# Optimization experiments

Hardware: AMD Instinct MI355X
Metric: run time of the kernel (lower is better)

## Reference

```python
import jax, jax.numpy as jnp
import numpy as np

T = 4096  # input sequence length; H = T - 16 after convs+pool


def setup_inputs() -> dict:
    key = jax.random.key(0)
    ks = jax.random.split(key, 20)
    def rn(k, shape, scale=0.05):
        return jax.random.normal(k, shape, dtype=jnp.float32) * scale
    return dict(
        evaluation=rn(ks[0], (T, 128), 1.0),
        template=rn(ks[1], (T, 128), 1.0),
        conv1_w=rn(ks[2], (16, 1, 5, 5)),  conv1_b=rn(ks[3], (16,)),
        conv2_w=rn(ks[4], (32, 16, 5, 5)), conv2_b=rn(ks[5], (32,)),
        conv3_w=rn(ks[6], (64, 32, 5, 5)), conv3_b=rn(ks[7], (64,)),
        lin1_w=rn(ks[8], (64, 3712)),      lin1_b=rn(ks[9], (64,)),
        gru_wih=rn(ks[10], (192, 64)),     gru_whh=rn(ks[11], (192, 64)),
        gru_bih=rn(ks[12], (192,)),        gru_bhh=rn(ks[13], (192,)),
        attn_w=rn(ks[14], (1, 64)),        attn_b=rn(ks[15], (1,)),
        lin3_w=rn(ks[16], (128, 64)),      lin3_b=rn(ks[17], (128,)),
        cls_w=rn(ks[18], (2, 128)),        cls_b=rn(ks[19], (2,)),
    )


def _conv(x, w, b):
    y = jax.lax.conv_general_dilated(x, w, (1, 1), 'VALID',
                                     dimension_numbers=('NCHW', 'OIHW', 'NCHW'))
    return y + b[None, :, None, None]


def _encode(x, c1w, c1b, c2w, c2b, c3w, c3b, l1w, l1b, wih, whh, bih, bhh):
    # x: (T, 128) -> (1, 1, T, 128); no activations between convs (as in source)
    x = x.reshape(1, 1, T, 128)
    x = _conv(x, c1w, c1b)   # (1,16,T-4,124)
    x = _conv(x, c2w, c2b)   # (1,32,T-8,120)
    x = _conv(x, c3w, c3b)   # (1,64,T-12,116)
    x = jax.lax.reduce_window(x, -jnp.inf, jax.lax.max,
                              (1, 1, 5, 2), (1, 1, 1, 2), 'VALID')  # (1,64,H,58)
    H = x.shape[2]
    # faithful raw reshape (channel-major flatten), same as torch.reshape
    x = x.reshape(H, 3712)
    x = x @ l1w.T + l1b      # (H, 64)
    # GRU (torch gate order r,z,n), h0 = 0; input gates precomputed
    gi = x @ wih.T + bih     # (H, 192)
    def step(h, gi_t):
        gh = whh @ h + bhh
        ir, iz, inn = jnp.split(gi_t, 3)
        hr, hz, hn = jnp.split(gh, 3)
        r = jax.nn.sigmoid(ir + hr)
        z = jax.nn.sigmoid(iz + hz)
        n = jnp.tanh(inn + r * hn)
        h_new = (1.0 - z) * n + z * h
        return h_new, h_new
    _, out = jax.lax.scan(step, jnp.zeros((64,), dtype=x.dtype), gi)
    return out               # (H, 64)


def reference(evaluation, template, conv1_w, conv1_b, conv2_w, conv2_b,
              conv3_w, conv3_b, lin1_w, lin1_b, gru_wih, gru_whh, gru_bih,
              gru_bhh, attn_w, attn_b, lin3_w, lin3_b, cls_w, cls_b):
    enc = lambda x: _encode(x, conv1_w, conv1_b, conv2_w, conv2_b, conv3_w,
                            conv3_b, lin1_w, lin1_b, gru_wih, gru_whh,
                            gru_bih, gru_bhh)
    e = enc(evaluation)      # (H, 64)
    t = enc(template)        # (H, 64)
    # alignment: aw[m,n] = <e_m, t_n>, softmax over dim 0 (m)
    aw = jax.nn.softmax(e @ t.T, axis=0)      # (H, H)
    t_prim = aw @ t                            # (H, 64)
    distance = jnp.abs(t_prim - e)             # (H, 64)
    attn = jax.nn.softmax((e @ attn_w.T + attn_b).ravel(), axis=0)  # (H,)
    # NOTE: source loops n over distance.size(dim=1)==64, i.e. only the first
    # 64 rows of distance / first 64 attention weights are used (replicated).
    D = distance.shape[1]
    representation = distance[:D].T @ attn[:D]  # (64,)
    out = jax.nn.relu(representation)
    out = jax.nn.relu(out @ lin3_w.T + lin3_b)
    return out @ cls_w.T + cls_b               # (2,)
```

## Files before the change

### kernel.cpp

```cpp
#include <hip/hip_runtime.h>
#include <hip/hip_fp16.h>

constexpr int T_IN = 4096, W_IN = 128;
constexpr int H1 = 4092, W1 = 124, C1 = 16;
constexpr int H2 = 4088, W2 = 120, C2 = 32;
constexpr int H3 = 4084, W3 = 116, C3 = 64;
constexpr int HP = 4080, WPW = 58;
constexpr int KF = 3712;

typedef float f32x16 __attribute__((ext_vector_type(16)));
typedef _Float16 f16x16 __attribute__((ext_vector_type(16)));
typedef _Float16 half2_t __attribute__((ext_vector_type(2)));

#define LOAD25(SRC, W) \
    float p00=(SRC)[0],        p01=(SRC)[1],        p02=(SRC)[2],        p03=(SRC)[3],        p04=(SRC)[4]; \
    float p10=(SRC)[(W)],      p11=(SRC)[(W)+1],    p12=(SRC)[(W)+2],    p13=(SRC)[(W)+3],    p14=(SRC)[(W)+4]; \
    float p20=(SRC)[2*(W)],    p21=(SRC)[2*(W)+1],  p22=(SRC)[2*(W)+2],  p23=(SRC)[2*(W)+3],  p24=(SRC)[2*(W)+4]; \
    float p30=(SRC)[3*(W)],    p31=(SRC)[3*(W)+1],  p32=(SRC)[3*(W)+2],  p33=(SRC)[3*(W)+3],  p34=(SRC)[3*(W)+4]; \
    float p40=(SRC)[4*(W)],    p41=(SRC)[4*(W)+1],  p42=(SRC)[4*(W)+2],  p43=(SRC)[4*(W)+3],  p44=(SRC)[4*(W)+4];

#define TAPS25(T) \
    T(p00, 0)  T(p01, 1)  T(p02, 2)  T(p03, 3)  T(p04, 4) \
    T(p10, 5)  T(p11, 6)  T(p12, 7)  T(p13, 8)  T(p14, 9) \
    T(p20,10)  T(p21,11)  T(p22,12)  T(p23,13)  T(p24,14) \
    T(p30,15)  T(p31,16)  T(p32,17)  T(p33,18)  T(p34,19) \
    T(p40,20)  T(p41,21)  T(p42,22)  T(p43,23)  T(p44,24)

#define KSTEP16(PK, WPTR) do { \
    const float4* w4_ = (const float4*)(WPTR); \
    float4 wA_ = w4_[0], wB_ = w4_[1], wC_ = w4_[2], wD_ = w4_[3]; \
    a0.x = fmaf((PK), wA_.x, a0.x); a0.y = fmaf((PK), wA_.y, a0.y); \
    a0.z = fmaf((PK), wA_.z, a0.z); a0.w = fmaf((PK), wA_.w, a0.w); \
    a1.x = fmaf((PK), wB_.x, a1.x); a1.y = fmaf((PK), wB_.y, a1.y); \
    a1.z = fmaf((PK), wB_.z, a1.z); a1.w = fmaf((PK), wB_.w, a1.w); \
    a2.x = fmaf((PK), wC_.x, a2.x); a2.y = fmaf((PK), wC_.y, a2.y); \
    a2.z = fmaf((PK), wC_.z, a2.z); a2.w = fmaf((PK), wC_.w, a2.w); \
    a3.x = fmaf((PK), wD_.x, a3.x); a3.y = fmaf((PK), wD_.y, a3.y); \
    a3.z = fmaf((PK), wD_.z, a3.z); a3.w = fmaf((PK), wD_.w, a3.w); \
} while (0)

__global__ __launch_bounds__(256, 2) void conv1_k(const float* __restrict__ x,
        const float* __restrict__ wp, const float* __restrict__ b,
        float* __restrict__ out) {
    int pos = blockIdx.x * 256 + threadIdx.x;
    if (pos >= H1 * W1) return;
    int h = pos / W1, wi = pos - h * W1;
    const float* src = x + h * W_IN + wi;
    const float4* b4 = (const float4*)b;
    float4 a0 = b4[0], a1 = b4[1], a2 = b4[2], a3 = b4[3];
    LOAD25(src, W_IN);
#define T1(P, K) KSTEP16(P, wp + (K) * 16);
    TAPS25(T1)
#undef T1
#pragma unroll
    for (int i = 0; i < 4; i++) {
        float4 v = (i == 0) ? a0 : (i == 1) ? a1 : (i == 2) ? a2 : a3;
        out[(size_t)(i * 4 + 0) * (H1 * W1) + pos] = v.x;
        out[(size_t)(i * 4 + 1) * (H1 * W1) + pos] = v.y;
        out[(size_t)(i * 4 + 2) * (H1 * W1) + pos] = v.z;
        out[(size_t)(i * 4 + 3) * (H1 * W1) + pos] = v.w;
    }
}

__global__ __launch_bounds__(256, 2) void conv2_k(const float* __restrict__ in,
        const float* __restrict__ wp, const float* __restrict__ b,
        float* __restrict__ out) {
    int pos = blockIdx.x * 256 + threadIdx.x;
    if (pos >= H2 * W2) return;
    int co0 = blockIdx.y * 16;
    int h = pos / W2, wi = pos - h * W2;
    const float4* b4 = (const float4*)(b + co0);
    float4 a0 = b4[0], a1 = b4[1], a2 = b4[2], a3 = b4[3];
#pragma unroll 1
    for (int ci = 0; ci < C1; ci++) {
        const float* src = in + (size_t)ci * (H1 * W1) + h * W1 + wi;
        const float* wb = wp + ci * 25 * C2 + co0;
        LOAD25(src, W1);
#define T2(P, K) KSTEP16(P, wb + (K) * C2);
        TAPS25(T2)
#undef T2
    }
#pragma unroll
    for (int i = 0; i < 4; i++) {
        float4 v = (i == 0) ? a0 : (i == 1) ? a1 : (i == 2) ? a2 : a3;
        out[(size_t)(co0 + i * 4 + 0) * (H2 * W2) + pos] = v.x;
        out[(size_t)(co0 + i * 4 + 1) * (H2 * W2) + pos] = v.y;
        out[(size_t)(co0 + i * 4 + 2) * (H2 * W2) + pos] = v.z;
        out[(size_t)(co0 + i * 4 + 3) * (H2 * W2) + pos] = v.w;
    }
}

__global__ __launch_bounds__(256, 2) void conv3_k(const float* __restrict__ in,
        const float* __restrict__ wp, const float* __restrict__ b,
        __half* __restrict__ out) {
    int pos = blockIdx.x * 256 + threadIdx.x;
    if (pos >= H3 * W3) return;
    int co0 = blockIdx.y * 16;
    int h = pos / W3, wi = pos - h * W3;
    const float4* b4 = (const float4*)(b + co0);
    float4 a0 = b4[0], a1 = b4[1], a2 = b4[2], a3 = b4[3];
#pragma unroll 1
    for (int ci = 0; ci < C2; ci++) {
        const float* src = in + (size_t)ci * (H2 * W2) + h * W2 + wi;
        const float* wb = wp + ci * 25 * C3 + co0;
        LOAD25(src, W2);
#define T3(P, K) KSTEP16(P, wb + (K) * C3);
        TAPS25(T3)
#undef T3
    }
#pragma unroll
    for (int i = 0; i < 4; i++) {
        float4 v = (i == 0) ? a0 : (i == 1) ? a1 : (i == 2) ? a2 : a3;
        out[(size_t)(co0 + i * 4 + 0) * (H3 * W3) + pos] = __float2half(v.x);
        out[(size_t)(co0 + i * 4 + 1) * (H3 * W3) + pos] = __float2half(v.y);
        out[(size_t)(co0 + i * 4 + 2) * (H3 * W3) + pos] = __float2half(v.z);
        out[(size_t)(co0 + i * 4 + 3) * (H3 * W3) + pos] = __float2half(v.w);
    }
}

__global__ __launch_bounds__(256) void pool_k(const __half* __restrict__ in,
        float* __restrict__ out) {
    int idx = blockIdx.x * 256 + threadIdx.x;
    if (idx >= C3 * HP * WPW) return;
    int w = idx % WPW; int rest = idx / WPW; int h = rest % HP; int c = rest / HP;
    const __half* base = in + (size_t)c * (H3 * W3) + (size_t)h * W3 + 2 * w;
    float m = -1e30f;
#pragma unroll
    for (int i = 0; i < 5; i++)
#pragma unroll
        for (int j = 0; j < 2; j++)
            m = fmaxf(m, __half2float(base[(size_t)i * W3 + j]));
    out[idx] = m;
}

__global__ __launch_bounds__(256, 2) void lin1_k(const float* __restrict__ X,
        const float* __restrict__ Wt, float* __restrict__ L) {
    __shared__ alignas(16) float Xs[64][68];
    int tid = threadIdx.x;
    int j = tid & 63, mg = tid >> 6;
    int m0 = blockIdx.x * 64;
    int c0 = blockIdx.y * 15;
    int c1 = (c0 + 15 < 58) ? c0 + 15 : 58;
    float4 la0 = {0.f,0.f,0.f,0.f}, la1 = la0, la2 = la0, la3 = la0;
    for (int cc = c0; cc < c1; cc++) {
        int k0 = cc * 64;
        __syncthreads();
#pragma unroll
        for (int tix = 0; tix < 16; tix++) {
            int idx = tid + tix * 256;
            int mm = idx >> 6, kk = idx & 63;
            int m = m0 + mm;
            Xs[kk][mm] = (m < HP) ? X[(size_t)m * KF + k0 + kk] : 0.f;
        }
        __syncthreads();
#pragma unroll 4
        for (int k = 0; k < 64; k++) {
            float wv = Wt[(size_t)(k0 + k) * 64 + j];
            const float4* xr = (const float4*)&Xs[k][mg * 16];
            float4 x0 = xr[0], x1 = xr[1], x2 = xr[2], x3 = xr[3];
            la0.x = fmaf(x0.x, wv, la0.x); la0.y = fmaf(x0.y, wv, la0.y);
            la0.z = fmaf(x0.z, wv, la0.z); la0.w = fmaf(x0.w, wv, la0.w);
            la1.x = fmaf(x1.x, wv, la1.x); la1.y = fmaf(x1.y, wv, la1.y);
            la1.z = fmaf(x1.z, wv, la1.z); la1.w = fmaf(x1.w, wv, la1.w);
            la2.x = fmaf(x2.x, wv, la2.x); la2.y = fmaf(x2.y, wv, la2.y);
            la2.z = fmaf(x2.z, wv, la2.z); la2.w = fmaf(x2.w, wv, la2.w);
            la3.x = fmaf(x3.x, wv, la3.x); la3.y = fmaf(x3.y, wv, la3.y);
            la3.z = fmaf(x3.z, wv, la3.z); la3.w = fmaf(x3.w, wv, la3.w);
        }
    }
    int mb = m0 + mg * 16;
#define LATOM(C, OFF) { int m = mb + (OFF); if (m < HP) atomicAdd(&L[(size_t)m * 64 + j], (C)); }
    LATOM(la0.x, 0)  LATOM(la0.y, 1)  LATOM(la0.z, 2)  LATOM(la0.w, 3)
    LATOM(la1.x, 4)  LATOM(la1.y, 5)  LATOM(la1.z, 6)  LATOM(la1.w, 7)
    LATOM(la2.x, 8)  LATOM(la2.y, 9)  LATOM(la2.z, 10) LATOM(la2.w, 11)
    LATOM(la3.x, 12) LATOM(la3.y, 13) LATOM(la3.z, 14) LATOM(la3.w, 15)
#undef LATOM
}

__global__ __launch_bounds__(192) void gi_k(const float* __restrict__ L,
        const float* __restrict__ wiht, const float* __restrict__ bc,
        float* __restrict__ gi) {
    __shared__ alignas(16) float Ls[8][64];
    int m0 = blockIdx.x * 8, g = threadIdx.x;
    for (int idx = g; idx < 512; idx += 192) {
        int r = idx >> 6, k = idx & 63;
        Ls[r][k] = L[(size_t)(m0 + r) * 64 + k];
    }
    __syncthreads();
    float bcv = bc[g];
#pragma unroll 1
    for (int r = 0; r < 8; r++) {
        float acc = bcv;
#pragma unroll
        for (int k = 0; k < 64; k++) acc = fmaf(Ls[r][k], wiht[k * 192 + g], acc);
        gi[(size_t)(m0 + r) * 192 + g] = acc;
    }
}

__global__ __launch_bounds__(192, 1) void gru_k(const float* __restrict__ gi0,
        const float* __restrict__ gi1, const _Float16* __restrict__ whh_h,
        const float* __restrict__ bhh, float* __restrict__ e,
        float* __restrict__ t) {
    const float* gi = blockIdx.x ? gi1 : gi0;
    float* out = blockIdx.x ? t : e;
    const int g = threadIdx.x;
    const f16x16* wp = (const f16x16*)(whh_h + (size_t)g * 64);
    f16x16 w0 = wp[0], w1 = wp[1], w2 = wp[2], w3 = wp[3];
    float bh = bhh[g];
    __shared__ alignas(64) _Float16 hs[64];
    __shared__ float Ax[192];
    const f16x16* hsv = (const f16x16*)hs;
    float h = 0.f;
    if (g < 64) hs[g] = (_Float16)0.f;
    __syncthreads();
    float p0 = 0.f, p1 = 0.f, p2 = 0.f;
    if (g < 64) { p0 = gi[g]; p1 = gi[64 + g]; p2 = gi[128 + g]; }
#define LGKM_BARRIER() do { \
    asm volatile("s_waitcnt lgkmcnt(0)" ::: "memory"); \
    __builtin_amdgcn_s_barrier(); \
    asm volatile("" ::: "memory"); \
} while (0)
#define DOT8(W, H, ACC) _Pragma("unroll") \
    for (int i_ = 0; i_ < 8; i_++) { \
        half2_t wa_; wa_[0] = (W)[2*i_]; wa_[1] = (W)[2*i_+1]; \
        half2_t ha_; ha_[0] = (H)[2*i_]; ha_[1] = (H)[2*i_+1]; \
        ACC = __builtin_amdgcn_fdot2(wa_, ha_, ACC, false); \
    }
#pragma unroll 1
    for (int m = 0; m < HP; m++) {
        f16x16 hv0 = hsv[0], hv1 = hsv[1], hv2 = hsv[2], hv3 = hsv[3];
        float c0 = p0, c1 = p1, c2 = p2;
        if (g < 64 && m + 1 < HP) {
            const float* gp = gi + (size_t)(m + 1) * 192;
            p0 = gp[g]; p1 = gp[64 + g]; p2 = gp[128 + g];
        }
        float a0 = 0.f, a1 = 0.f, a2 = 0.f, a3 = 0.f;
        DOT8(w0, hv0, a0)
        DOT8(w1, hv1, a1)
        DOT8(w2, hv2, a2)
        DOT8(w3, hv3, a3)
        float a = (a0 + a1) + (a2 + a3) + bh;
        Ax[g] = a;
        LGKM_BARRIER();
        if (g < 64) {
            float az = Ax[64 + g], an = Ax[128 + g];
            float rg = 1.f / (1.f + __expf(-(c0 + a)));
            float zg = 1.f / (1.f + __expf(-(c1 + az)));
            float pre = c2 + rg * an;
            float ex = __expf(2.f * pre);
            float nn = 1.f - 2.f / (ex + 1.f);
            h = (1.f - zg) * nn + zg * h;
            hs[g] = (_Float16)h;
            out[(size_t)m * 64 + g] = h;
        }
        LGKM_BARRIER();
    }
#undef DOT8
#undef LGKM_BARRIER
}

__global__ __launch_bounds__(256) void astat_k(const float* __restrict__ e,
        const float* __restrict__ t, float* __restrict__ pM,
        float* __restrict__ pZ) {
    __shared__ alignas(16) float Ts[64][68];
    __shared__ float Ms[4][64], Zs[4][64];
    int tid = threadIdx.x;
    int nl = tid & 63, ms = tid >> 6;
    int n0 = blockIdx.x * 64;
#pragma unroll
    for (int i = 0; i < 16; i++) {
        int idx = tid + i * 256;
        int rr = idx >> 6, kk = idx & 63;
        int n = n0 + rr;
        Ts[rr][kk] = (n < HP) ? t[(size_t)n * 64 + kk] : 0.f;
    }
    __syncthreads();
    float M = -1e30f, Z = 0.f;
    int m0 = blockIdx.y * 510;
    const float4* Trow = (const float4*)&Ts[nl][0];
    for (int m = m0 + ms; m < m0 + 510; m += 4) {
        const float4* er = (const float4*)(e + (size_t)m * 64);
        float a0 = 0, a1 = 0, a2 = 0, a3 = 0;
#pragma unroll
        for (int i = 0; i < 16; i++) {
            float4 evv = er[i], tv = Trow[i];
            a0 = fmaf(evv.x, tv.x, a0); a1 = fmaf(evv.y, tv.y, a1);
            a2 = fmaf(evv.z, tv.z, a2); a3 = fmaf(evv.w, tv.w, a3);
        }
        float s = (a0 + a1) + (a2 + a3);
        float nM = fmaxf(M, s);
        Z = Z * __expf(M - nM) + __expf(s - nM);
        M = nM;
    }
    Ms[ms][nl] = M; Zs[ms][nl] = Z;
    __syncthreads();
    if (ms == 0) {
#pragma unroll
        for (int i = 1; i < 4; i++) {
            float m2 = Ms[i][nl], z2 = Zs[i][nl];
            float nM = fmaxf(M, m2);
            Z = Z * __expf(M - nM) + z2 * __expf(m2 - nM);
            M = nM;
        }
        int n = n0 + nl;
        if (n < HP) { pM[(size_t)blockIdx.y * HP + n] = M; pZ[(size_t)blockIdx.y * HP + n] = Z; }
    }
}

__global__ __launch_bounds__(256) void attnlog_k(const float* __restrict__ e,
        const float* __restrict__ aw, const float* __restrict__ ab,
        float* __restrict__ alog) {
    int m = blockIdx.x * 256 + threadIdx.x;
    if (m >= HP) return;
    float acc = ab[0];
    const float4* er = (const float4*)(e + (size_t)m * 64);
    const float4* ar = (const float4*)aw;
#pragma unroll
    for (int i = 0; i < 16; i++) {
        float4 evv = er[i], av = ar[i];
        acc += evv.x * av.x + evv.y * av.y + evv.z * av.z + evv.w * av.w;
    }
    alog[m] = acc;
}

__global__ __launch_bounds__(256) void reduce_k(const float* __restrict__ pM,
        const float* __restrict__ pZ, float* __restrict__ Mn,
        float* __restrict__ Zn, const float* __restrict__ alog,
        float* __restrict__ scal) {
    int tid = threadIdx.x;
    if (blockIdx.x < 16) {
        int n = blockIdx.x * 256 + tid;
        if (n >= HP) return;
        float M = pM[n], Z = pZ[n];
#pragma unroll
        for (int y = 1; y < 8; y++) {
            float m2 = pM[(size_t)y * HP + n], z2 = pZ[(size_t)y * HP + n];
            float nM = fmaxf(M, m2);
            Z = Z * __expf(M - nM) + z2 * __expf(m2 - nM);
            M = nM;
        }
        Mn[n] = M; Zn[n] = Z;
    } else {
        __shared__ float red[256];
        float m = -1e30f;
        for (int i = tid; i < HP; i += 256) m = fmaxf(m, alog[i]);
        red[tid] = m; __syncthreads();
        for (int s = 128; s > 0; s >>= 1) {
            if (tid < s) red[tid] = fmaxf(red[tid], red[tid + s]);
            __syncthreads();
        }
        float Ma = red[0]; __syncthreads();
        float z = 0.f;
        for (int i = tid; i < HP; i += 256) z += __expf(alog[i] - Ma);
        red[tid] = z; __syncthreads();
        for (int s = 128; s > 0; s >>= 1) {
            if (tid < s) red[tid] += red[tid + s];
            __syncthreads();
        }
        if (tid == 0) { scal[0] = Ma; scal[1] = red[0]; }
    }
}

__global__ __launch_bounds__(256) void wmat_k(const float* __restrict__ e,
        const float* __restrict__ t, const float* __restrict__ Mn,
        const float* __restrict__ Zn, float* __restrict__ Wm) {
    __shared__ alignas(16) float Es[64][68];
    int tid = threadIdx.x;
#pragma unroll
    for (int i = 0; i < 16; i++) {
        int idx = tid + i * 256;
        int rr = idx >> 6, kk = idx & 63;
        Es[rr][kk] = e[(size_t)rr * 64 + kk];
    }
    __syncthreads();
    int n = blockIdx.x * 256 + tid;
    if (n >= HP) return;
    float tn[64];
    const float4* tr = (const float4*)(t + (size_t)n * 64);
    float4* tn4 = (float4*)tn;
#pragma unroll
    for (int i = 0; i < 16; i++) tn4[i] = tr[i];
    float mM = Mn[n], iZ = 1.f / Zn[n];
#pragma unroll 1
    for (int m = 0; m < 64; m++) {
        const float4* Er = (const float4*)&Es[m][0];
        float a0 = 0, a1 = 0, a2 = 0, a3 = 0;
#pragma unroll
        for (int i = 0; i < 16; i++) {
            float4 evv = Er[i], tv = tn4[i];
            a0 = fmaf(evv.x, tv.x, a0); a1 = fmaf(evv.y, tv.y, a1);
            a2 = fmaf(evv.z, tv.z, a2); a3 = fmaf(evv.w, tv.w, a3);
        }
        float s = (a0 + a1) + (a2 + a3);
        Wm[(size_t)m * HP + n] = __expf(s - mM) * iZ;
    }
}

__global__ __launch_bounds__(256) void tprim_k(const float* __restrict__ Wm,
        const float* __restrict__ t, float* __restrict__ tp) {
    __shared__ float Ws[64][64];
    __shared__ float Ts[64][64];
    int tid = threadIdx.x;
    int n0 = blockIdx.x * 64;
#pragma unroll
    for (int i = 0; i < 16; i++) {
        int idx = tid + i * 256;
        int r = idx >> 6, c = idx & 63;
        Ws[r][c] = (n0 + c < HP) ? Wm[(size_t)r * HP + n0 + c] : 0.f;
        Ts[r][c] = (n0 + r < HP) ? t[(size_t)(n0 + r) * 64 + c] : 0.f;
    }
    __syncthreads();
    int d = tid & 63, mg = tid >> 6;
    float acc[16];
#pragma unroll
    for (int i = 0; i < 16; i++) acc[i] = 0.f;
    for (int k = 0; k < 64; k++) {
        float tv = Ts[k][d];
#pragma unroll
        for (int mm = 0; mm < 16; mm++) acc[mm] = fmaf(Ws[mg * 16 + mm][k], tv, acc[mm]);
    }
#pragma unroll
    for (int mm = 0; mm < 16; mm++)
        atomicAdd(&tp[(size_t)(mg * 16 + mm) * 64 + d], acc[mm]);
}

__global__ __launch_bounds__(256) void final_k(const float* __restrict__ tp,
        const float* __restrict__ e, const float* __restrict__ alog,
        const float* __restrict__ scal, const float* __restrict__ l3w,
        const float* __restrict__ l3b, const float* __restrict__ cw,
        const float* __restrict__ cb, float* __restrict__ out) {
    __shared__ float r1[64], hid[128];
    int tid = threadIdx.x;
    float Ma = scal[0], iZa = 1.f / scal[1];
    if (tid < 64) {
        float acc = 0.f;
        for (int m = 0; m < 64; m++) {
            float a = __expf(alog[m] - Ma) * iZa;
            acc += fabsf(tp[m * 64 + tid] - e[m * 64 + tid]) * a;
        }
        r1[tid] = fmaxf(acc, 0.f);
    }
    __syncthreads();
    if (tid < 128) {
        float acc = l3b[tid];
        for (int d = 0; d < 64; d++) acc = fmaf(r1[d], l3w[tid * 64 + d], acc);
        hid[tid] = fmaxf(acc, 0.f);
    }
    __syncthreads();
    if (tid < 2) {
        float acc = cb[tid];
        for (int j = 0; j < 128; j++) acc = fmaf(hid[j], cw[tid * 128 + j], acc);
        out[tid] = acc;
    }
}

__global__ __launch_bounds__(256) void transpose_l1w_k(const float* __restrict__ w,
        float* __restrict__ wt) {
    int idx = blockIdx.x * 256 + threadIdx.x;
    if (idx >= KF * 64) return;
    int k = idx >> 6, j = idx & 63;
    wt[idx] = w[(size_t)j * KF + k];
}
__global__ __launch_bounds__(256) void pack_w1_k(const float* __restrict__ w,
        float* __restrict__ wp) {
    int idx = blockIdx.x * 256 + threadIdx.x;
    if (idx >= 400) return;
    int k = idx >> 4, co = idx & 15;
    wp[idx] = w[co * 25 + k];
}
__global__ __launch_bounds__(256) void pack_w2_k(const float* __restrict__ w,
        float* __restrict__ wp) {
    int idx = blockIdx.x * 256 + threadIdx.x;
    if (idx >= 12800) return;
    int co = idx & 31, rest = idx >> 5;
    wp[idx] = w[co * 400 + rest];
}
__global__ __launch_bounds__(256) void pack_w3_k(const float* __restrict__ w,
        float* __restrict__ wp) {
    int idx = blockIdx.x * 256 + threadIdx.x;
    if (idx >= 51200) return;
    int co = idx & 63, rest = idx >> 6;
    wp[idx] = w[co * 800 + rest];
}
__global__ __launch_bounds__(256) void pack_wih_k(const float* __restrict__ wih,
        const float* __restrict__ bih, const float* __restrict__ l1b,
        const float* __restrict__ whh, float* __restrict__ wiht,
        float* __restrict__ bc, _Float16* __restrict__ whh_h) {
    int idx = blockIdx.x * 256 + threadIdx.x;
    if (idx < 12288) {
        int g = idx % 192, k = idx / 192;
        wiht[idx] = wih[g * 64 + k];
        whh_h[idx] = (_Float16)whh[idx];
    }
    if (idx < 192) {
        float acc = bih[idx];
#pragma unroll
        for (int k = 0; k < 64; k++) acc = fmaf(wih[idx * 64 + k], l1b[k], acc);
        bc[idx] = acc;
    }
}

extern "C" void kernel_launch(void* const* d_in, const int* in_sizes, int n_in,
                              void* d_out, int out_size, void* d_ws, size_t ws_size,
                              hipStream_t stream) {
    const float* ev    = (const float*)d_in[0];
    const float* tmpl  = (const float*)d_in[1];
    const float* w1    = (const float*)d_in[2];
    const float* b1    = (const float*)d_in[3];
    const float* w2    = (const float*)d_in[4];
    const float* b2    = (const float*)d_in[5];
    const float* w3    = (const float*)d_in[6];
    const float* b3    = (const float*)d_in[7];
    const float* l1w   = (const float*)d_in[8];
    const float* l1b   = (const float*)d_in[9];
    const float* wih   = (const float*)d_in[10];
    const float* whh   = (const float*)d_in[11];
    const float* bih   = (const float*)d_in[12];
    const float* bhh   = (const float*)d_in[13];
    const float* aw    = (const float*)d_in[14];
    const float* ab    = (const float*)d_in[15];
    const float* l3w   = (const float*)d_in[16];
    const float* l3b   = (const float*)d_in[17];
    const float* cw    = (const float*)d_in[18];
    const float* cb    = (const float*)d_in[19];
    float* out = (float*)d_out;
    (void)in_sizes; (void)n_in; (void)out_size;

    char* ws = (char*)d_ws;
    size_t off = 0;
    auto alloc = [&](size_t bytes) -> char* {
        char* p = ws + off;
        off += (bytes + 255) & ~(size_t)255;
        return p;
    };
    size_t szA = (size_t)C3 * H3 * W3 * 2;
    size_t szA1 = (size_t)C1 * H1 * W1 * 4;
    if (szA1 > szA) szA = szA1;
    char*  A    = alloc(szA);
    float* B    = (float*)alloc((size_t)C2 * H2 * W2 * 4);
    float* Wt   = (float*)alloc((size_t)KF * 64 * 4);
    float* w1p  = (float*)alloc(400 * 4);
    float* w2p  = (float*)alloc(12800 * 4);
    float* w3p  = (float*)alloc(51200 * 4);
    float* wiht = (float*)alloc(12288 * 4);
    _Float16* whhh = (_Float16*)alloc(12288 * 2);
    float* bc   = (float*)alloc(256 * 4);
    float* L    = (float*)alloc((size_t)HP * 64 * 4);
    float* gi0  = (float*)alloc((size_t)HP * 192 * 4);
    float* gi1  = (float*)alloc((size_t)HP * 192 * 4);
    float* ebuf = (float*)alloc((size_t)HP * 64 * 4);
    float* tbuf = (float*)alloc((size_t)HP * 64 * 4);
    float* pM   = (float*)alloc((size_t)8 * HP * 4);
    float* pZ   = (float*)alloc((size_t)8 * HP * 4);
    float* Mn   = (float*)alloc(HP * 4);
    float* Zn   = (float*)alloc(HP * 4);
    float* Wm   = (float*)alloc((size_t)64 * HP * 4);
    float* alog = (float*)alloc(HP * 4);
    float* tpm  = (float*)alloc(64 * 64 * 4);
    float* scal = (float*)alloc(256);
    if (off > ws_size) return;

    transpose_l1w_k<<<dim3((KF * 64 + 255) / 256), dim3(256), 0, stream>>>(l1w, Wt);
    pack_w1_k<<<dim3(2), dim3(256), 0, stream>>>(w1, w1p);
    pack_w2_k<<<dim3(50), dim3(256), 0, stream>>>(w2, w2p);
    pack_w3_k<<<dim3(200), dim3(256), 0, stream>>>(w3, w3p);
    pack_wih_k<<<dim3(48), dim3(256), 0, stream>>>(wih, bih, l1b, whh, wiht, bc, whhh);

    for (int bsel = 0; bsel < 2; bsel++) {
        const float* xin = bsel ? tmpl : ev;
        float* gib = bsel ? gi1 : gi0;
        conv1_k<<<dim3((H1 * W1 + 255) / 256), dim3(256), 0, stream>>>(xin, w1p, b1, (float*)A);
        conv2_k<<<dim3((H2 * W2 + 255) / 256, 2), dim3(256), 0, stream>>>((const float*)A, w2p, b2, B);
        conv3_k<<<dim3((H3 * W3 + 255) / 256, 4), dim3(256), 0, stream>>>(B, w3p, b3, (__half*)A);
        pool_k<<<dim3((C3 * HP * WPW + 255) / 256), dim3(256), 0, stream>>>((const __half*)A, B);
        hipMemsetAsync(L, 0, (size_t)HP * 64 * 4, stream);
        lin1_k<<<dim3(64, 4), dim3(256), 0, stream>>>(B, Wt, L);
        gi_k<<<dim3(HP / 8), dim3(192), 0, stream>>>(L, wiht, bc, gib);
    }
    gru_k<<<dim3(2), dim3(192), 0, stream>>>(gi0, gi1, whhh, bhh, ebuf, tbuf);
    astat_k<<<dim3(64, 8), dim3(256), 0, stream>>>(ebuf, tbuf, pM, pZ);
    attnlog_k<<<dim3(16), dim3(256), 0, stream>>>(ebuf, aw, ab, alog);
    reduce_k<<<dim3(17), dim3(256), 0, stream>>>(pM, pZ, Mn, Zn, alog, scal);
    wmat_k<<<dim3(16), dim3(256), 0, stream>>>(ebuf, tbuf, Mn, Zn, Wm);
    hipMemsetAsync(tpm, 0, 64 * 64 * 4, stream);
    tprim_k<<<dim3(64), dim3(256), 0, stream>>>(Wm, tbuf, tpm);
    final_k<<<dim3(1), dim3(256), 0, stream>>>(tpm, ebuf, alog, scal, l3w, l3b, cw, cb, out);
}
```

Baseline: 3.749 ms.

## Use fp16 activations and packed fdot2 for conv2 and conv3

Conv1 and conv2 now write their outputs as fp16 instead of fp32, which halves the intermediate traffic. Conv2 and conv3 read fp16 inputs and fp16 weights packed in pairs of taps (padded from 25 to 26), and accumulate in fp32 with v_dot2 instructions. This is meant to halve both the FMA instruction count and the memory bandwidth of the dominant conv stages. It costs precision on intermediate activations and weights, and adds per-element conversion and pair-packing work in registers.

```diff
diff --git a/kernel.cpp b/kernel.cpp
--- a/kernel.cpp
+++ b/kernel.cpp
@@ -39,9 +39,51 @@
     a3.z = fmaf((PK), wD_.z, a3.z); a3.w = fmaf((PK), wD_.w, a3.w); \
 } while (0)
 
+#define LOAD25H(SRC, W) \
+    _Float16 q00=(_Float16)(SRC)[0],      q01=(_Float16)(SRC)[1],      q02=(_Float16)(SRC)[2],      q03=(_Float16)(SRC)[3],      q04=(_Float16)(SRC)[4]; \
+    _Float16 q10=(_Float16)(SRC)[(W)],    q11=(_Float16)(SRC)[(W)+1],  q12=(_Float16)(SRC)[(W)+2],  q13=(_Float16)(SRC)[(W)+3],  q14=(_Float16)(SRC)[(W)+4]; \
+    _Float16 q20=(_Float16)(SRC)[2*(W)],  q21=(_Float16)(SRC)[2*(W)+1],q22=(_Float16)(SRC)[2*(W)+2],q23=(_Float16)(SRC)[2*(W)+3],q24=(_Float16)(SRC)[2*(W)+4]; \
+    _Float16 q30=(_Float16)(SRC)[3*(W)],  q31=(_Float16)(SRC)[3*(W)+1],q32=(_Float16)(SRC)[3*(W)+2],q33=(_Float16)(SRC)[3*(W)+3],q34=(_Float16)(SRC)[3*(W)+4]; \
+    _Float16 q40=(_Float16)(SRC)[4*(W)],  q41=(_Float16)(SRC)[4*(W)+1],q42=(_Float16)(SRC)[4*(W)+2],q43=(_Float16)(SRC)[4*(W)+3],q44=(_Float16)(SRC)[4*(W)+4];
+
+#define MKPAIRS() \
+    half2_t P0, P1, P2, P3, P4, P5, P6, P7, P8, P9, P10, P11, P12; \
+    P0[0]=q00; P0[1]=q01;  P1[0]=q02; P1[1]=q03;  P2[0]=q04; P2[1]=q10; \
+    P3[0]=q11; P3[1]=q12;  P4[0]=q13; P4[1]=q14;  P5[0]=q20; P5[1]=q21; \
+    P6[0]=q22; P6[1]=q23;  P7[0]=q24; P7[1]=q30;  P8[0]=q31; P8[1]=q32; \
+    P9[0]=q33; P9[1]=q34;  P10[0]=q40; P10[1]=q41; P11[0]=q42; P11[1]=q43; \
+    P12[0]=q44; P12[1]=(_Float16)0.f;
+
+#define DSTEP16(PH, WPTR) do { \
+    const half2_t* wv_ = (const half2_t*)(WPTR); \
+    a0.x = __builtin_amdgcn_fdot2((PH), wv_[0],  a0.x, false); \
+    a0.y = __builtin_amdgcn_fdot2((PH), wv_[1],  a0.y, false); \
+    a0.z = __builtin_amdgcn_fdot2((PH), wv_[2],  a0.z, false); \
+    a0.w = __builtin_amdgcn_fdot2((PH), wv_[3],  a0.w, false); \
+    a1.x = __builtin_amdgcn_fdot2((PH), wv_[4],  a1.x, false); \
+    a1.y = __builtin_amdgcn_fdot2((PH), wv_[5],  a1.y, false); \
+    a1.z = __builtin_amdgcn_fdot2((PH), wv_[6],  a1.z, false); \
+    a1.w = __builtin_amdgcn_fdot2((PH), wv_[7],  a1.w, false); \
+    a2.x = __builtin_amdgcn_fdot2((PH), wv_[8],  a2.x, false); \
+    a2.y = __builtin_amdgcn_fdot2((PH), wv_[9],  a2.y, false); \
+    a2.z = __builtin_amdgcn_fdot2((PH), wv_[10], a2.z, false); \
+    a2.w = __builtin_amdgcn_fdot2((PH), wv_[11], a2.w, false); \
+    a3.x = __builtin_amdgcn_fdot2((PH), wv_[12], a3.x, false); \
+    a3.y = __builtin_amdgcn_fdot2((PH), wv_[13], a3.y, false); \
+    a3.z = __builtin_amdgcn_fdot2((PH), wv_[14], a3.z, false); \
+    a3.w = __builtin_amdgcn_fdot2((PH), wv_[15], a3.w, false); \
+} while (0)
+
+#define PAIRS13(D, CI, CS, WB) \
+    D(P0,  ((CI)*13+ 0)) D(P1,  ((CI)*13+ 1)) D(P2,  ((CI)*13+ 2)) \
+    D(P3,  ((CI)*13+ 3)) D(P4,  ((CI)*13+ 4)) D(P5,  ((CI)*13+ 5)) \
+    D(P6,  ((CI)*13+ 6)) D(P7,  ((CI)*13+ 7)) D(P8,  ((CI)*13+ 8)) \
+    D(P9,  ((CI)*13+ 9)) D(P10, ((CI)*13+10)) D(P11, ((CI)*13+11)) \
+    D(P12, ((CI)*13+12))
+
 __global__ __launch_bounds__(256, 2) void conv1_k(const float* __restrict__ x,
         const float* __restrict__ wp, const float* __restrict__ b,
-        float* __restrict__ out) {
+        __half* __restrict__ out) {
     int pos = blockIdx.x * 256 + threadIdx.x;
     if (pos >= H1 * W1) return;
     int h = pos / W1, wi = pos - h * W1;
@@ -55,16 +97,16 @@
 #pragma unroll
     for (int i = 0; i < 4; i++) {
         float4 v = (i == 0) ? a0 : (i == 1) ? a1 : (i == 2) ? a2 : a3;
-        out[(size_t)(i * 4 + 0) * (H1 * W1) + pos] = v.x;
-        out[(size_t)(i * 4 + 1) * (H1 * W1) + pos] = v.y;
-        out[(size_t)(i * 4 + 2) * (H1 * W1) + pos] = v.z;
-        out[(size_t)(i * 4 + 3) * (H1 * W1) + pos] = v.w;
-    }
-}
-
-__global__ __launch_bounds__(256, 2) void conv2_k(const float* __restrict__ in,
-        const float* __restrict__ wp, const float* __restrict__ b,
-        float* __restrict__ out) {
+        out[(size_t)(i * 4 + 0) * (H1 * W1) + pos] = __float2half(v.x);
+        out[(size_t)(i * 4 + 1) * (H1 * W1) + pos] = __float2half(v.y);
+        out[(size_t)(i * 4 + 2) * (H1 * W1) + pos] = __float2half(v.z);
+        out[(size_t)(i * 4 + 3) * (H1 * W1) + pos] = __float2half(v.w);
+    }
+}
+
+__global__ __launch_bounds__(256, 2) void conv2_k(const __half* __restrict__ in,
+        const _Float16* __restrict__ wp2, const float* __restrict__ b,
+        __half* __restrict__ out) {
     int pos = blockIdx.x * 256 + threadIdx.x;
     if (pos >= H2 * W2) return;
     int co0 = blockIdx.y * 16;
@@ -73,25 +115,25 @@
     float4 a0 = b4[0], a1 = b4[1], a2 = b4[2], a3 = b4[3];
 #pragma unroll 1
     for (int ci = 0; ci < C1; ci++) {
-        const float* src = in + (size_t)ci * (H1 * W1) + h * W1 + wi;
-        const float* wb = wp + ci * 25 * C2 + co0;
-        LOAD25(src, W1);
-#define T2(P, K) KSTEP16(P, wb + (K) * C2);
-        TAPS25(T2)
-#undef T2
+        const __half* src = in + (size_t)ci * (H1 * W1) + h * W1 + wi;
+        LOAD25H(src, W1);
+        MKPAIRS();
+#define D2(PH, QI) DSTEP16(PH, wp2 + ((size_t)(QI) * C2 + co0) * 2);
+        PAIRS13(D2, ci, C2, wp2)
+#undef D2
     }
 #pragma unroll
     for (int i = 0; i < 4; i++) {
         float4 v = (i == 0) ? a0 : (i == 1) ? a1 : (i == 2) ? a2 : a3;
-        out[(size_t)(co0 + i * 4 + 0) * (H2 * W2) + pos] = v.x;
-        out[(size_t)(co0 + i * 4 + 1) * (H2 * W2) + pos] = v.y;
-        out[(size_t)(co0 + i * 4 + 2) * (H2 * W2) + pos] = v.z;
-        out[(size_t)(co0 + i * 4 + 3) * (H2 * W2) + pos] = v.w;
-    }
-}
-
-__global__ __launch_bounds__(256, 2) void conv3_k(const float* __restrict__ in,
-        const float* __restrict__ wp, const float* __restrict__ b,
+        out[(size_t)(co0 + i * 4 + 0) * (H2 * W2) + pos] = __float2half(v.x);
+        out[(size_t)(co0 + i * 4 + 1) * (H2 * W2) + pos] = __float2half(v.y);
+        out[(size_t)(co0 + i * 4 + 2) * (H2 * W2) + pos] = __float2half(v.z);
+        out[(size_t)(co0 + i * 4 + 3) * (H2 * W2) + pos] = __float2half(v.w);
+    }
+}
+
+__global__ __launch_bounds__(256, 2) void conv3_k(const __half* __restrict__ in,
+        const _Float16* __restrict__ wp2, const float* __restrict__ b,
         __half* __restrict__ out) {
     int pos = blockIdx.x * 256 + threadIdx.x;
     if (pos >= H3 * W3) return;
@@ -101,12 +143,12 @@
     float4 a0 = b4[0], a1 = b4[1], a2 = b4[2], a3 = b4[3];
 #pragma unroll 1
     for (int ci = 0; ci < C2; ci++) {
-        const float* src = in + (size_t)ci * (H2 * W2) + h * W2 + wi;
-        const float* wb = wp + ci * 25 * C3 + co0;
-        LOAD25(src, W2);
-#define T3(P, K) KSTEP16(P, wb + (K) * C3);
-        TAPS25(T3)
-#undef T3
+        const __half* src = in + (size_t)ci * (H2 * W2) + h * W2 + wi;
+        LOAD25H(src, W2);
+        MKPAIRS();
+#define D3(PH, QI) DSTEP16(PH, wp2 + ((size_t)(QI) * C3 + co0) * 2);
+        PAIRS13(D3, ci, C3, wp2)
+#undef D3
     }
 #pragma unroll
     for (int i = 0; i < 4; i++) {
@@ -468,19 +510,29 @@
     int k = idx >> 4, co = idx & 15;
     wp[idx] = w[co * 25 + k];
 }
-__global__ __launch_bounds__(256) void pack_w2_k(const float* __restrict__ w,
-        float* __restrict__ wp) {
+__global__ __launch_bounds__(256) void pack_w2p_k(const float* __restrict__ w,
+        _Float16* __restrict__ wp2) {
     int idx = blockIdx.x * 256 + threadIdx.x;
-    if (idx >= 12800) return;
-    int co = idx & 31, rest = idx >> 5;
-    wp[idx] = w[co * 400 + rest];
-}
-__global__ __launch_bounds__(256) void pack_w3_k(const float* __restrict__ w,
-        float* __restrict__ wp) {
+    if (idx >= 16 * 13 * 32) return;
+    int co = idx & 31; int rest = idx >> 5;
+    int q = rest % 13, ci = rest / 13;
+    int t0 = 2 * q, t1 = 2 * q + 1;
+    float v0 = (t0 < 25) ? w[co * 400 + ci * 25 + t0] : 0.f;
+    float v1 = (t1 < 25) ? w[co * 400 + ci * 25 + t1] : 0.f;
+    wp2[(size_t)idx * 2 + 0] = (_Float16)v0;
+    wp2[(size_t)idx * 2 + 1] = (_Float16)v1;
+}
+__global__ __launch_bounds__(256) void pack_w3p_k(const float* __restrict__ w,
+        _Float16* __restrict__ wp2) {
     int idx = blockIdx.x * 256 + threadIdx.x;
-    if (idx >= 51200) return;
-    int co = idx & 63, rest = idx >> 6;
-    wp[idx] = w[co * 800 + rest];
+    if (idx >= 32 * 13 * 64) return;
+    int co = idx & 63; int rest = idx >> 6;
+    int q = rest % 13, ci = rest / 13;
+    int t0 = 2 * q, t1 = 2 * q + 1;
+    float v0 = (t0 < 25) ? w[co * 800 + ci * 25 + t0] : 0.f;
+    float v1 = (t1 < 25) ? w[co * 800 + ci * 25 + t1] : 0.f;
+    wp2[(size_t)idx * 2 + 0] = (_Float16)v0;
+    wp2[(size_t)idx * 2 + 1] = (_Float16)v1;
 }
 __global__ __launch_bounds__(256) void pack_wih_k(const float* __restrict__ wih,
         const float* __restrict__ bih, const float* __restrict__ l1b,
@@ -534,14 +586,12 @@
         return p;
     };
     size_t szA = (size_t)C3 * H3 * W3 * 2;
-    size_t szA1 = (size_t)C1 * H1 * W1 * 4;
-    if (szA1 > szA) szA = szA1;
     char*  A    = alloc(szA);
-    float* B    = (float*)alloc((size_t)C2 * H2 * W2 * 4);
+    float* B    = (float*)alloc((size_t)HP * KF * 4);
     float* Wt   = (float*)alloc((size_t)KF * 64 * 4);
     float* w1p  = (float*)alloc(400 * 4);
-    float* w2p  = (float*)alloc(12800 * 4);
-    float* w3p  = (float*)alloc(51200 * 4);
+    _Float16* w2p2 = (_Float16*)alloc(16 * 13 * 32 * 2 * 2);
+    _Float16* w3p2 = (_Float16*)alloc(32 * 13 * 64 * 2 * 2);
     float* wiht = (float*)alloc(12288 * 4);
     _Float16* whhh = (_Float16*)alloc(12288 * 2);
     float* bc   = (float*)alloc(256 * 4);
@@ -562,16 +612,16 @@
 
     transpose_l1w_k<<<dim3((KF * 64 + 255) / 256), dim3(256), 0, stream>>>(l1w, Wt);
     pack_w1_k<<<dim3(2), dim3(256), 0, stream>>>(w1, w1p);
-    pack_w2_k<<<dim3(50), dim3(256), 0, stream>>>(w2, w2p);
-    pack_w3_k<<<dim3(200), dim3(256), 0, stream>>>(w3, w3p);
+    pack_w2p_k<<<dim3((16 * 13 * 32 + 255) / 256), dim3(256), 0, stream>>>(w2, w2p2);
+    pack_w3p_k<<<dim3((32 * 13 * 64 + 255) / 256), dim3(256), 0, stream>>>(w3, w3p2);
     pack_wih_k<<<dim3(48), dim3(256), 0, stream>>>(wih, bih, l1b, whh, wiht, bc, whhh);
 
     for (int bsel = 0; bsel < 2; bsel++) {
         const float* xin = bsel ? tmpl : ev;
         float* gib = bsel ? gi1 : gi0;
-        conv1_k<<<dim3((H1 * W1 + 255) / 256), dim3(256), 0, stream>>>(xin, w1p, b1, (float*)A);
-        conv2_k<<<dim3((H2 * W2 + 255) / 256, 2), dim3(256), 0, stream>>>((const float*)A, w2p, b2, B);
-        conv3_k<<<dim3((H3 * W3 + 255) / 256, 4), dim3(256), 0, stream>>>(B, w3p, b3, (__half*)A);
+        conv1_k<<<dim3((H1 * W1 + 255) / 256), dim3(256), 0, stream>>>(xin, w1p, b1, (__half*)A);
+        conv2_k<<<dim3((H2 * W2 + 255) / 256, 2), dim3(256), 0, stream>>>((const __half*)A, w2p2, b2, (__half*)B);
+        conv3_k<<<dim3((H3 * W3 + 255) / 256, 4), dim3(256), 0, stream>>>((const __half*)B, w3p2, b3, (__half*)A);
         pool_k<<<dim3((C3 * HP * WPW + 255) / 256), dim3(256), 0, stream>>>((const __half*)A, B);
         hipMemsetAsync(L, 0, (size_t)HP * 64 * 4, stream);
         lin1_k<<<dim3(64, 4), dim3(256), 0, stream>>>(B, Wt, L);
```

Measured after the change: 3.671 ms. 2.1% less time.
